# Performance work log

Measured on AMD Instinct MI355X. Metric: run time of the kernel, lower is better.

## Reference

```python
import jax, jax.numpy as jnp
import numpy as np

B, S, E, H, DK = 2, 2048, 2048, 16, 128


def _make_freq_pos_enc(dim, max_seq_len):
    # matches torch freq_pos_enc: interleaved repeat '(f r)' with r=2
    inv_freq = 1.0 / (10000.0 ** (jnp.arange(0, dim, 2, dtype=jnp.float32) / dim))
    pos = jnp.arange(max_seq_len, dtype=jnp.float32)
    pe = pos[:, None] * inv_freq[None, :]          # [S, dim/2]
    return jnp.repeat(pe, 2, axis=-1)              # [S, dim], interleaved


def setup_inputs() -> dict:
    key = jax.random.key(0)
    ks = jax.random.split(key, 5)
    sc = 1.0 / np.sqrt(E)
    return {
        "x": jax.random.normal(ks[0], (B, S, E), jnp.float32),
        "wq": jax.random.normal(ks[1], (H * DK, E), jnp.float32) * sc,
        "wk": jax.random.normal(ks[2], (H * DK, E), jnp.float32) * sc,
        "wv": jax.random.normal(ks[3], (H * DK, E), jnp.float32) * sc,
        "wo": jax.random.normal(ks[4], (E, H * DK), jnp.float32) * sc,
        "freq_pos_enc": _make_freq_pos_enc(DK, S),
        "num_heads": H,
        "d_k": DK,
    }


def rotate_half(u):
    # interleaved pairs: (d r) with r=2 -> (-u2, u1) interleaved back
    shp = u.shape
    u = u.reshape(shp[:-1] + (shp[-1] // 2, 2))
    u1, u2 = u[..., 0], u[..., 1]
    return jnp.stack((-u2, u1), axis=-1).reshape(shp)


def reference(x, wq, wk, wv, wo, freq_pos_enc, num_heads, d_k):
    b, s, _ = x.shape

    def proj(w):  # [B,S,E] @ [E, H*DK] -> [B,H,S,DK]
        return (x @ w.T).reshape(b, s, num_heads, d_k).transpose(0, 2, 1, 3)

    q, k, v = proj(wq), proj(wk), proj(wv)

    pe = freq_pos_enc[:s]                           # [S, DK]
    cos, sin = jnp.cos(pe), jnp.sin(pe)
    rot = lambda u: u * cos + rotate_half(u) * sin  # broadcast over [B,H]
    q, k = rot(q), rot(k)

    scale = 1.0 / jnp.sqrt(jnp.asarray(d_k, x.dtype))
    scores = jnp.einsum('bhqd,bhkd->bhqk', q, k) * scale
    causal = jnp.tril(jnp.ones((s, s), bool))
    scores = jnp.where(causal, scores, jnp.finfo(scores.dtype).min)
    attn = jnp.einsum('bhqk,bhkd->bhqd', jax.nn.softmax(scores, axis=-1), v)

    out = attn.transpose(0, 2, 1, 3).reshape(b, s, num_heads * d_k)
    return out @ wo.T
```

## Files before the change

### kernel.cpp

```cpp
#include <hip/hip_runtime.h>
#include <hip/hip_bf16.h>

typedef __attribute__((ext_vector_type(8))) short bf16x8;
typedef __attribute__((ext_vector_type(4))) float f32x4;
typedef unsigned short u16;
typedef unsigned int u32;

#define B_ 2
#define S_ 2048
#define E_ 2048
#define H_ 16
#define DK_ 128
#define QSCALE_ 0.12751741f
#define THR2_ 11.5415603f

#define MFMA16(a,b,c) __builtin_amdgcn_mfma_f32_16x16x32_bf16((a),(b),(c),0,0,0)
#define GLD16(g, l) __builtin_amdgcn_global_load_lds((const __attribute__((address_space(1))) void*)(g), (__attribute__((address_space(3))) void*)(l), 16, 0, 0)

__device__ __forceinline__ float b2f(short s) {
    u32 u = ((u32)(u16)s) << 16;
    float f; __builtin_memcpy(&f, &u, 4); return f;
}

__global__ void cast_all(const float* __restrict__ x,
                         const float* __restrict__ w0, const float* __restrict__ w1,
                         const float* __restrict__ w2, const float* __restrict__ w3,
                         __hip_bfloat16* __restrict__ xo,
                         __hip_bfloat16* __restrict__ o0, __hip_bfloat16* __restrict__ o1,
                         __hip_bfloat16* __restrict__ o2, __hip_bfloat16* __restrict__ o3,
                         const float* __restrict__ pe, float* __restrict__ ct,
                         float* __restrict__ st,
                         int nx4, int nw4) {
    int i = blockIdx.x * blockDim.x + threadIdx.x;
    const int y = blockIdx.y;
    const float* in; __hip_bfloat16* out; int n4;
    if (y == 0)      { in = x;  out = xo; n4 = nx4; }
    else if (y == 1) { in = w0; out = o0; n4 = nw4; }
    else if (y == 2) { in = w1; out = o1; n4 = nw4; }
    else if (y == 3) { in = w2; out = o2; n4 = nw4; }
    else             { in = w3; out = o3; n4 = nw4; }
    if (i < n4) {
        float4 v = ((const float4*)in)[i];
        __hip_bfloat16 ob[4] = {__float2bfloat16(v.x), __float2bfloat16(v.y),
                                __float2bfloat16(v.z), __float2bfloat16(v.w)};
        ushort4 u; __builtin_memcpy(&u, ob, 8);
        ((ushort4*)out)[i] = u;
    }
    if (y == 0 && blockIdx.x < (S_ * 64 / 256)) {
        int t = blockIdx.x * 256 + threadIdx.x;
        int s = t >> 6, d2 = t & 63;
        float ang = pe[(size_t)s * DK_ + 2 * d2];
        ct[t] = cosf(ang);
        st[t] = sinf(ang);
    }
}

__global__ __launch_bounds__(256, 2)
void gemm_qkv(const __hip_bfloat16* __restrict__ X,
              const __hip_bfloat16* __restrict__ WQ, const __hip_bfloat16* __restrict__ WK,
              const __hip_bfloat16* __restrict__ WV,
              __hip_bfloat16* __restrict__ Qo, __hip_bfloat16* __restrict__ Ko,
              __hip_bfloat16* __restrict__ Vo,
              const float* __restrict__ CT, const float* __restrict__ ST)
{
    __shared__ __align__(16) __hip_bfloat16 As[128 * 64];
    __shared__ __align__(16) __hip_bfloat16 Bs[128 * 64];
    const int tid = threadIdx.x;
    const int lane = tid & 63, wv = tid >> 6;
    const int wr = wv >> 1, wc = wv & 1;
    const int which = blockIdx.y >> 4;
    const __hip_bfloat16* W = which == 0 ? WQ : which == 1 ? WK : WV;
    const int m0 = blockIdx.x * 128, n0 = (blockIdx.y & 15) * 128;
    const int g = lane >> 4, c = lane & 15;
    const int K = E_;

    f32x4 acc[4][4];
    #pragma unroll
    for (int i = 0; i < 4; ++i)
        #pragma unroll
        for (int j = 0; j < 4; ++j) acc[i][j] = f32x4{0.f, 0.f, 0.f, 0.f};

    for (int k0 = 0; k0 < K; k0 += 64) {
        __syncthreads();
        #pragma unroll
        for (int it = 0; it < 4; ++it) {
            int o = (it * 256 + tid) * 16;
            int row = o >> 7;
            int colb = (o ^ ((row & 7) << 4)) & 127;
            GLD16((const char*)(X + (size_t)(m0 + row) * K + k0) + colb, (char*)As + o);
            GLD16((const char*)(W + (size_t)(n0 + row) * K + k0) + colb, (char*)Bs + o);
        }
        __syncthreads();
        #pragma unroll
        for (int ks = 0; ks < 2; ++ks) {
            bf16x8 af[4], bfm[4];
            #pragma unroll
            for (int i = 0; i < 4; ++i) {
                int arow = wr * 64 + i * 16 + c;
                int ab = arow * 128 + ((ks * 64 + g * 16) ^ ((arow & 7) << 4));
                af[i] = *(const bf16x8*)((const char*)As + ab);
                int brow = wc * 64 + i * 16 + c;
                int bb = brow * 128 + ((ks * 64 + g * 16) ^ ((brow & 7) << 4));
                bfm[i] = *(const bf16x8*)((const char*)Bs + bb);
            }
            #pragma unroll
            for (int i = 0; i < 4; ++i)
                #pragma unroll
                for (int j = 0; j < 4; ++j)
                    acc[i][j] = MFMA16(af[i], bfm[j], acc[i][j]);
        }
    }

    if (which < 2) {
        __hip_bfloat16* Cq = which == 0 ? Qo : Ko;
        const float qsc = (which == 0) ? QSCALE_ : 1.0f;
        #pragma unroll
        for (int i = 0; i < 4; ++i)
            #pragma unroll
            for (int j = 0; j < 4; ++j)
                #pragma unroll
                for (int r = 0; r < 4; ++r) {
                    float v = acc[i][j][r];
                    float vp = __shfl_xor(v, 1);
                    int m = m0 + wr * 64 + i * 16 + 4 * g + r;
                    int n = n0 + wc * 64 + j * 16 + c;
                    int srow = m & (S_ - 1), d = n & (DK_ - 1);
                    float cs = CT[srow * 64 + (d >> 1)] * qsc;
                    float sn = ST[srow * 64 + (d >> 1)] * qsc;
                    float o = (c & 1) ? __builtin_fmaf(v, cs, vp * sn)
                                      : __builtin_fmaf(v, cs, -vp * sn);
                    size_t a = ((size_t)((m >> 11) * 16 + (n >> 7)) * S_ + srow) * DK_ + d;
                    Cq[a] = __float2bfloat16(o);
                }
    } else {
        #pragma unroll
        for (int i = 0; i < 4; ++i)
            #pragma unroll
            for (int j = 0; j < 4; ++j) {
                int m = m0 + wr * 64 + i * 16 + 4 * g;
                int n = n0 + wc * 64 + j * 16 + c;
                int s0 = m & (S_ - 1), d = n & (DK_ - 1);
                __hip_bfloat16 ob[4];
                #pragma unroll
                for (int r = 0; r < 4; ++r) ob[r] = __float2bfloat16(acc[i][j][r]);
                ushort4 u; __builtin_memcpy(&u, ob, 8);
                size_t a = ((size_t)((m >> 11) * 16 + (n >> 7)) * DK_ + d) * S_ + s0;
                *(ushort4*)(Vo + a) = u;
            }
    }
}

__global__ __launch_bounds__(256, 2)
void gemm_out(const __hip_bfloat16* __restrict__ A, const __hip_bfloat16* __restrict__ W,
              float* __restrict__ Cout, int M, int N, int K)
{
    __shared__ __align__(16) __hip_bfloat16 As[128 * 64];
    __shared__ __align__(16) __hip_bfloat16 Bs[128 * 64];
    const int tid = threadIdx.x;
    const int lane = tid & 63, wv = tid >> 6;
    const int wr = wv >> 1, wc = wv & 1;
    const int m0 = blockIdx.x * 128, n0 = blockIdx.y * 128;
    const int g = lane >> 4, c = lane & 15;

    f32x4 acc[4][4];
    #pragma unroll
    for (int i = 0; i < 4; ++i)
        #pragma unroll
        for (int j = 0; j < 4; ++j) acc[i][j] = f32x4{0.f, 0.f, 0.f, 0.f};

    for (int k0 = 0; k0 < K; k0 += 64) {
        __syncthreads();
        #pragma unroll
        for (int it = 0; it < 4; ++it) {
            int o = (it * 256 + tid) * 16;
            int row = o >> 7;
            int colb = (o ^ ((row & 7) << 4)) & 127;
            GLD16((const char*)(A + (size_t)(m0 + row) * K + k0) + colb, (char*)As + o);
            GLD16((const char*)(W + (size_t)(n0 + row) * K + k0) + colb, (char*)Bs + o);
        }
        __syncthreads();
        #pragma unroll
        for (int ks = 0; ks < 2; ++ks) {
            bf16x8 af[4], bfm[4];
            #pragma unroll
            for (int i = 0; i < 4; ++i) {
                int arow = wr * 64 + i * 16 + c;
                int ab = arow * 128 + ((ks * 64 + g * 16) ^ ((arow & 7) << 4));
                af[i] = *(const bf16x8*)((const char*)As + ab);
                int brow = wc * 64 + i * 16 + c;
                int bb = brow * 128 + ((ks * 64 + g * 16) ^ ((brow & 7) << 4));
                bfm[i] = *(const bf16x8*)((const char*)Bs + bb);
            }
            #pragma unroll
            for (int i = 0; i < 4; ++i)
                #pragma unroll
                for (int j = 0; j < 4; ++j)
                    acc[i][j] = MFMA16(af[i], bfm[j], acc[i][j]);
        }
    }

    #pragma unroll
    for (int i = 0; i < 4; ++i)
        #pragma unroll
        for (int j = 0; j < 4; ++j)
            #pragma unroll
            for (int r = 0; r < 4; ++r) {
                int m = m0 + wr * 64 + i * 16 + 4 * g + r;
                int n = n0 + wc * 64 + j * 16 + c;
                Cout[(size_t)m * N + n] = acc[i][j][r];
            }
}

__device__ __forceinline__ void stage_kv(const __hip_bfloat16* Kp, const __hip_bfloat16* Vp,
                                         char* ks, char* vs, int kv0, int tid) {
    #pragma unroll
    for (int it = 0; it < 4; ++it) {
        int o = (it * 256 + tid) * 16;
        int row = o >> 8;
        int cb = (o ^ ((row & 7) << 4)) & 255;
        GLD16((const char*)(Kp + (size_t)(kv0 + row) * DK_) + cb, ks + o);
    }
    #pragma unroll
    for (int it = 0; it < 4; ++it) {
        int o = (it * 256 + tid) * 16;
        int row = o >> 7;
        int cb = (o ^ ((row & 7) << 4)) & 127;
        GLD16((const char*)(Vp + (size_t)row * S_ + kv0) + cb, vs + o);
    }
}

__global__ __launch_bounds__(256, 2)
void attn_kernel(const __hip_bfloat16* __restrict__ Q,
                 const __hip_bfloat16* __restrict__ Kt,
                 const __hip_bfloat16* __restrict__ VT,
                 __hip_bfloat16* __restrict__ O)
{
    __shared__ __align__(16) __hip_bfloat16 Ks[2][64 * 128];
    __shared__ __align__(16) __hip_bfloat16 Vs[2][128 * 64];
    __shared__ __align__(16) __hip_bfloat16 Ps[4][16 * 72];

    const int tid = threadIdx.x, lane = tid & 63, w = tid >> 6;
    const int g = lane >> 4, c = lane & 15;
    const int id = blockIdx.x;
    const int slot = id & 7, jj = id >> 3;
    const int bh = ((jj >> 4) << 3) | slot;
    const int xq = jj & 15;
    const int b = bh >> 4, h = bh & 15;
    const size_t base_bh = (size_t)bh * S_ * DK_;
    const __hip_bfloat16* Qp = Q + base_bh;
    const __hip_bfloat16* Kp = Kt + base_bh;
    const __hip_bfloat16* Vp = VT + base_bh;

    #pragma unroll 1
    for (int pass = 0; pass < 2; ++pass) {
        const int qt = pass ? (31 - xq) : xq;
        const int qw = qt * 64 + w * 16;
        const int ntiles = qt + 1;

        bf16x8 qf[4];
        #pragma unroll
        for (int ds = 0; ds < 4; ++ds)
            qf[ds] = *(const bf16x8*)(Qp + (size_t)(qw + c) * DK_ + ds * 32 + g * 8);

        f32x4 oacc[8];
        #pragma unroll
        for (int fd = 0; fd < 8; ++fd) oacc[fd] = f32x4{0.f, 0.f, 0.f, 0.f};
        float M[4], Lp[4];
        #pragma unroll
        for (int r = 0; r < 4; ++r) { M[r] = -1e30f; Lp[r] = 0.f; }

        stage_kv(Kp, Vp, (char*)Ks[0], (char*)Vs[0], 0, tid);
        __syncthreads();

        int cur = 0;
        for (int t = 0; t < ntiles; ++t) {
            const int kv0 = t * 64;
            if (t + 1 < ntiles)
                stage_kv(Kp, Vp, (char*)Ks[cur ^ 1], (char*)Vs[cur ^ 1], kv0 + 64, tid);

            const bool diag = (kv0 + 63 > qw);

            f32x4 sacc[4];
            #pragma unroll
            for (int f = 0; f < 4; ++f) sacc[f] = f32x4{0.f, 0.f, 0.f, 0.f};
            #pragma unroll
            for (int f = 0; f < 4; ++f) {
                #pragma unroll
                for (int ds = 0; ds < 4; ++ds) {
                    int krow = f * 16 + c;
                    int kbyt = krow * 256 + ((ds * 64 + g * 16) ^ ((krow & 7) << 4));
                    bf16x8 kf = *(const bf16x8*)((const char*)Ks[cur] + kbyt);
                    sacc[f] = MFMA16(qf[ds], kf, sacc[f]);
                }
            }

            float p[4][4];
            float mt[4] = {-1e30f, -1e30f, -1e30f, -1e30f};
            #pragma unroll
            for (int f = 0; f < 4; ++f)
                #pragma unroll
                for (int r = 0; r < 4; ++r) {
                    float v = sacc[f][r];
                    if (diag && (kv0 + f * 16 + c > qw + 4 * g + r)) v = -1e30f;
                    p[f][r] = v;
                    mt[r] = fmaxf(mt[r], v);
                }
            bool grow = (mt[0] > M[0] + THR2_) || (mt[1] > M[1] + THR2_) ||
                        (mt[2] > M[2] + THR2_) || (mt[3] > M[3] + THR2_);
            if (__any(grow)) {
                float al[4];
                #pragma unroll
                for (int r = 0; r < 4; ++r) {
                    float v = mt[r];
                    v = fmaxf(v, __shfl_xor(v, 1));
                    v = fmaxf(v, __shfl_xor(v, 2));
                    v = fmaxf(v, __shfl_xor(v, 4));
                    v = fmaxf(v, __shfl_xor(v, 8));
                    float mn = fmaxf(M[r], v);
                    al[r] = exp2f(M[r] - mn);
                    M[r] = mn;
                    Lp[r] *= al[r];
                }
                #pragma unroll
                for (int fd = 0; fd < 8; ++fd)
                    #pragma unroll
                    for (int r = 0; r < 4; ++r) oacc[fd][r] *= al[r];
            }
            #pragma unroll
            for (int f = 0; f < 4; ++f)
                #pragma unroll
                for (int r = 0; r < 4; ++r) {
                    float e = exp2f(p[f][r] - M[r]);
                    Lp[r] += e;
                    Ps[w][(4 * g + r) * 72 + f * 16 + c] = __float2bfloat16(e);
                }

            #pragma unroll
            for (int ks2 = 0; ks2 < 2; ++ks2) {
                bf16x8 pf = *(const bf16x8*)&Ps[w][c * 72 + ks2 * 32 + g * 8];
                #pragma unroll
                for (int fd = 0; fd < 8; ++fd) {
                    int vrow = fd * 16 + c;
                    int vb = vrow * 128 + ((ks2 * 64 + g * 16) ^ ((vrow & 7) << 4));
                    bf16x8 vf = *(const bf16x8*)((const char*)Vs[cur] + vb);
                    oacc[fd] = MFMA16(pf, vf, oacc[fd]);
                }
            }
            __syncthreads();
            cur ^= 1;
        }

        float rl[4];
        #pragma unroll
        for (int r = 0; r < 4; ++r) {
            float v = Lp[r];
            v += __shfl_xor(v, 1);
            v += __shfl_xor(v, 2);
            v += __shfl_xor(v, 4);
            v += __shfl_xor(v, 8);
            rl[r] = 1.0f / v;
        }
        #pragma unroll
        for (int fd = 0; fd < 8; ++fd) {
            #pragma unroll
            for (int r = 0; r < 4; ++r) {
                int s = qw + 4 * g + r;
                size_t a = ((size_t)(b * S_ + s)) * (H_ * DK_) + h * DK_ + fd * 16 + c;
                O[a] = __float2bfloat16(oacc[fd][r] * rl[r]);
            }
        }
    }
}

extern "C" void kernel_launch(void* const* d_in, const int* in_sizes, int n_in,
                              void* d_out, int out_size, void* d_ws, size_t ws_size,
                              hipStream_t stream) {
    const float* x  = (const float*)d_in[0];
    const float* wq = (const float*)d_in[1];
    const float* wk = (const float*)d_in[2];
    const float* wv = (const float*)d_in[3];
    const float* wo = (const float*)d_in[4];
    const float* pe = (const float*)d_in[5];
    float* out = (float*)d_out;

    const size_t XE = (size_t)B_ * S_ * E_;
    const size_t WE = (size_t)E_ * H_ * DK_;
    __hip_bfloat16* xb  = (__hip_bfloat16*)d_ws;
    __hip_bfloat16* wqb = xb + XE;
    __hip_bfloat16* wkb = wqb + WE;
    __hip_bfloat16* wvb = wkb + WE;
    __hip_bfloat16* wob = wvb + WE;
    __hip_bfloat16* qb  = wob + WE;
    __hip_bfloat16* kb  = qb + XE;
    __hip_bfloat16* vT  = kb + XE;
    __hip_bfloat16* at  = vT + XE;
    float* ct = (float*)(at + XE);
    float* st = ct + (size_t)S_ * 64;

    cast_all<<<dim3((int)(XE / 4 / 256), 5), 256, 0, stream>>>(
        x, wq, wk, wv, wo, xb, wqb, wkb, wvb, wob, pe, ct, st,
        (int)(XE / 4), (int)(WE / 4));

    gemm_qkv<<<dim3(32, 48), 256, 0, stream>>>(xb, wqb, wkb, wvb, qb, kb, vT, ct, st);

    attn_kernel<<<dim3(512), 256, 0, stream>>>(qb, kb, vT, at);

    gemm_out<<<dim3(32, 16), 256, 0, stream>>>(at, wob, out, B_ * S_, E_, H_ * DK_);
}
```

Baseline: 259.6 us.

## Process both paired causal query tiles in one shared KV sweep

The attention kernel used to run two sequential passes per block, one for query tile xq and one for 31-xq, each streaming its own K/V tiles from global memory. Now it keeps two sets of Q fragments, accumulators and softmax state, and makes a single pass over the K/V tiles of the longer row. The short tile's work runs only while it is still active, so K/V global loads and block barriers for the short tile's range are shared. The cost is roughly double the live accumulator and Q registers, which raises register pressure and could cause spills or lower occupancy.

```diff
diff --git a/kernel.cpp b/kernel.cpp
--- a/kernel.cpp
+++ b/kernel.cpp
@@ -229,6 +229,64 @@
     }
 }
 
+__device__ __forceinline__ void softmax_pv(const f32x4* sacc, float* M, float* Lp,
+                                           f32x4* oacc, const char* Vc,
+                                           __hip_bfloat16* Psw,
+                                           int qw, int kv0, int g, int c, bool diag)
+{
+    float p[4][4];
+    float mt[4] = {-1e30f, -1e30f, -1e30f, -1e30f};
+    #pragma unroll
+    for (int f = 0; f < 4; ++f)
+        #pragma unroll
+        for (int r = 0; r < 4; ++r) {
+            float v = sacc[f][r];
+            if (diag && (kv0 + f * 16 + c > qw + 4 * g + r)) v = -1e30f;
+            p[f][r] = v;
+            mt[r] = fmaxf(mt[r], v);
+        }
+    bool grow = (mt[0] > M[0] + THR2_) || (mt[1] > M[1] + THR2_) ||
+                (mt[2] > M[2] + THR2_) || (mt[3] > M[3] + THR2_);
+    if (__any(grow)) {
+        float al[4];
+        #pragma unroll
+        for (int r = 0; r < 4; ++r) {
+            float v = mt[r];
+            v = fmaxf(v, __shfl_xor(v, 1));
+            v = fmaxf(v, __shfl_xor(v, 2));
+            v = fmaxf(v, __shfl_xor(v, 4));
+            v = fmaxf(v, __shfl_xor(v, 8));
+            float mn = fmaxf(M[r], v);
+            al[r] = exp2f(M[r] - mn);
+            M[r] = mn;
+            Lp[r] *= al[r];
+        }
+        #pragma unroll
+        for (int fd = 0; fd < 8; ++fd)
+            #pragma unroll
+            for (int r = 0; r < 4; ++r) oacc[fd][r] *= al[r];
+    }
+    #pragma unroll
+    for (int f = 0; f < 4; ++f)
+        #pragma unroll
+        for (int r = 0; r < 4; ++r) {
+            float e = exp2f(p[f][r] - M[r]);
+            Lp[r] += e;
+            Psw[(4 * g + r) * 72 + f * 16 + c] = __float2bfloat16(e);
+        }
+    #pragma unroll
+    for (int ks2 = 0; ks2 < 2; ++ks2) {
+        bf16x8 pf = *(const bf16x8*)&Psw[c * 72 + ks2 * 32 + g * 8];
+        #pragma unroll
+        for (int fd = 0; fd < 8; ++fd) {
+            int vrow = fd * 16 + c;
+            int vb = vrow * 128 + ((ks2 * 64 + g * 16) ^ ((vrow & 7) << 4));
+            bf16x8 vf = *(const bf16x8*)(Vc + vb);
+            oacc[fd] = MFMA16(pf, vf, oacc[fd]);
+        }
+    }
+}
+
 __global__ __launch_bounds__(256, 2)
 void attn_kernel(const __hip_bfloat16* __restrict__ Q,
                  const __hip_bfloat16* __restrict__ Kt,
@@ -250,110 +308,82 @@
     const __hip_bfloat16* Qp = Q + base_bh;
     const __hip_bfloat16* Kp = Kt + base_bh;
     const __hip_bfloat16* Vp = VT + base_bh;
-
-    #pragma unroll 1
-    for (int pass = 0; pass < 2; ++pass) {
-        const int qt = pass ? (31 - xq) : xq;
-        const int qw = qt * 64 + w * 16;
-        const int ntiles = qt + 1;
-
-        bf16x8 qf[4];
-        #pragma unroll
-        for (int ds = 0; ds < 4; ++ds)
-            qf[ds] = *(const bf16x8*)(Qp + (size_t)(qw + c) * DK_ + ds * 32 + g * 8);
-
-        f32x4 oacc[8];
-        #pragma unroll
-        for (int fd = 0; fd < 8; ++fd) oacc[fd] = f32x4{0.f, 0.f, 0.f, 0.f};
-        float M[4], Lp[4];
-        #pragma unroll
-        for (int r = 0; r < 4; ++r) { M[r] = -1e30f; Lp[r] = 0.f; }
-
-        stage_kv(Kp, Vp, (char*)Ks[0], (char*)Vs[0], 0, tid);
-        __syncthreads();
-
-        int cur = 0;
-        for (int t = 0; t < ntiles; ++t) {
-            const int kv0 = t * 64;
-            if (t + 1 < ntiles)
-                stage_kv(Kp, Vp, (char*)Ks[cur ^ 1], (char*)Vs[cur ^ 1], kv0 + 64, tid);
-
-            const bool diag = (kv0 + 63 > qw);
-
-            f32x4 sacc[4];
-            #pragma unroll
-            for (int f = 0; f < 4; ++f) sacc[f] = f32x4{0.f, 0.f, 0.f, 0.f};
-            #pragma unroll
-            for (int f = 0; f < 4; ++f) {
+    __hip_bfloat16* Psw = Ps[w];
+
+    const int qt1 = xq, qt2 = 31 - xq;
+    const int qw1 = qt1 * 64 + w * 16, qw2 = qt2 * 64 + w * 16;
+    const int tmax = qt2 + 1;
+
+    bf16x8 qf1[4], qf2[4];
+    #pragma unroll
+    for (int ds = 0; ds < 4; ++ds) {
+        qf1[ds] = *(const bf16x8*)(Qp + (size_t)(qw1 + c) * DK_ + ds * 32 + g * 8);
+        qf2[ds] = *(const bf16x8*)(Qp + (size_t)(qw2 + c) * DK_ + ds * 32 + g * 8);
+    }
+
+    f32x4 o1[8], o2[8];
+    #pragma unroll
+    for (int fd = 0; fd < 8; ++fd) { o1[fd] = f32x4{0.f,0.f,0.f,0.f}; o2[fd] = f32x4{0.f,0.f,0.f,0.f}; }
+    float M1[4], L1[4], M2[4], L2[4];
+    #pragma unroll
+    for (int r = 0; r < 4; ++r) { M1[r] = -1e30f; L1[r] = 0.f; M2[r] = -1e30f; L2[r] = 0.f; }
+
+    stage_kv(Kp, Vp, (char*)Ks[0], (char*)Vs[0], 0, tid);
+    __syncthreads();
+
+    int cur = 0;
+    for (int t = 0; t < tmax; ++t) {
+        const int kv0 = t * 64;
+        if (t + 1 < tmax)
+            stage_kv(Kp, Vp, (char*)Ks[cur ^ 1], (char*)Vs[cur ^ 1], kv0 + 64, tid);
+
+        const char* Kc = (const char*)Ks[cur];
+        const char* Vc = (const char*)Vs[cur];
+        const bool act1 = (t <= qt1);
+
+        f32x4 s1[4], s2[4];
+        if (act1) {
+            #pragma unroll
+            for (int f = 0; f < 4; ++f) s1[f] = f32x4{0.f,0.f,0.f,0.f};
+            #pragma unroll
+            for (int f = 0; f < 4; ++f)
                 #pragma unroll
                 for (int ds = 0; ds < 4; ++ds) {
                     int krow = f * 16 + c;
                     int kbyt = krow * 256 + ((ds * 64 + g * 16) ^ ((krow & 7) << 4));
-                    bf16x8 kf = *(const bf16x8*)((const char*)Ks[cur] + kbyt);
-                    sacc[f] = MFMA16(qf[ds], kf, sacc[f]);
+                    bf16x8 kf = *(const bf16x8*)(Kc + kbyt);
+                    s1[f] = MFMA16(qf1[ds], kf, s1[f]);
                 }
-            }
-
-            float p[4][4];
-            float mt[4] = {-1e30f, -1e30f, -1e30f, -1e30f};
-            #pragma unroll
-            for (int f = 0; f < 4; ++f)
-                #pragma unroll
-                for (int r = 0; r < 4; ++r) {
-                    float v = sacc[f][r];
-                    if (diag && (kv0 + f * 16 + c > qw + 4 * g + r)) v = -1e30f;
-                    p[f][r] = v;
-                    mt[r] = fmaxf(mt[r], v);
-                }
-            bool grow = (mt[0] > M[0] + THR2_) || (mt[1] > M[1] + THR2_) ||
-                        (mt[2] > M[2] + THR2_) || (mt[3] > M[3] + THR2_);
-            if (__any(grow)) {
-                float al[4];
-                #pragma unroll
-                for (int r = 0; r < 4; ++r) {
-                    float v = mt[r];
-                    v = fmaxf(v, __shfl_xor(v, 1));
-                    v = fmaxf(v, __shfl_xor(v, 2));
-                    v = fmaxf(v, __shfl_xor(v, 4));
-                    v = fmaxf(v, __shfl_xor(v, 8));
-                    float mn = fmaxf(M[r], v);
-                    al[r] = exp2f(M[r] - mn);
-                    M[r] = mn;
-                    Lp[r] *= al[r];
-                }
-                #pragma unroll
-                for (int fd = 0; fd < 8; ++fd)
-                    #pragma unroll
-                    for (int r = 0; r < 4; ++r) oacc[fd][r] *= al[r];
-            }
-            #pragma unroll
-            for (int f = 0; f < 4; ++f)
-                #pragma unroll
-                for (int r = 0; r < 4; ++r) {
-                    float e = exp2f(p[f][r] - M[r]);
-                    Lp[r] += e;
-                    Ps[w][(4 * g + r) * 72 + f * 16 + c] = __float2bfloat16(e);
-                }
-
-            #pragma unroll
-            for (int ks2 = 0; ks2 < 2; ++ks2) {
-                bf16x8 pf = *(const bf16x8*)&Ps[w][c * 72 + ks2 * 32 + g * 8];
-                #pragma unroll
-                for (int fd = 0; fd < 8; ++fd) {
-                    int vrow = fd * 16 + c;
-                    int vb = vrow * 128 + ((ks2 * 64 + g * 16) ^ ((vrow & 7) << 4));
-                    bf16x8 vf = *(const bf16x8*)((const char*)Vs[cur] + vb);
-                    oacc[fd] = MFMA16(pf, vf, oacc[fd]);
-                }
-            }
-            __syncthreads();
-            cur ^= 1;
-        }
-
+        }
+        #pragma unroll
+        for (int f = 0; f < 4; ++f) s2[f] = f32x4{0.f,0.f,0.f,0.f};
+        #pragma unroll
+        for (int f = 0; f < 4; ++f)
+            #pragma unroll
+            for (int ds = 0; ds < 4; ++ds) {
+                int krow = f * 16 + c;
+                int kbyt = krow * 256 + ((ds * 64 + g * 16) ^ ((krow & 7) << 4));
+                bf16x8 kf = *(const bf16x8*)(Kc + kbyt);
+                s2[f] = MFMA16(qf2[ds], kf, s2[f]);
+            }
+
+        if (act1)
+            softmax_pv(s1, M1, L1, o1, Vc, Psw, qw1, kv0, g, c, (kv0 + 63 > qw1));
+        softmax_pv(s2, M2, L2, o2, Vc, Psw, qw2, kv0, g, c, (kv0 + 63 > qw2));
+
+        __syncthreads();
+        cur ^= 1;
+    }
+
+    #pragma unroll
+    for (int q = 0; q < 2; ++q) {
+        const float* Lq = q == 0 ? L1 : L2;
+        const f32x4* oq = q == 0 ? o1 : o2;
+        const int qw = q == 0 ? qw1 : qw2;
         float rl[4];
         #pragma unroll
         for (int r = 0; r < 4; ++r) {
-            float v = Lp[r];
+            float v = Lq[r];
             v += __shfl_xor(v, 1);
             v += __shfl_xor(v, 2);
             v += __shfl_xor(v, 4);
@@ -366,7 +396,7 @@
             for (int r = 0; r < 4; ++r) {
                 int s = qw + 4 * g + r;
                 size_t a = ((size_t)(b * S_ + s)) * (H_ * DK_) + h * DK_ + fd * 16 + c;
-                O[a] = __float2bfloat16(oacc[fd][r] * rl[r]);
+                O[a] = __float2bfloat16(oq[fd][r] * rl[r]);
             }
         }
     }
```

Measured after the change: 271.2 us. 4.5% more time.
